# Kernel optimization log

Measured on AMD Instinct MI355X. Metric: run time of the kernel, lower is better.

The kernel has to match this reference:

```python
import jax, jax.numpy as jnp
import numpy as np

N_HEADS = 16
D_QK = 64
D_MODEL = 1024
LN_EPS = 1e-6
B, QL, KVL = 2, 2048, 2048


def rms_norm(x, weight, eps=LN_EPS):
    var = jnp.mean(jnp.square(x.astype(jnp.float32)), axis=-1, keepdims=True)
    return (x * jax.lax.rsqrt(var + eps)).astype(x.dtype) * weight


def setup_inputs() -> dict:
    key = jax.random.key(0)
    ks = jax.random.split(key, 5)
    scale_h = 1.0 / np.sqrt(D_MODEL)
    return {
        "q_hidden_states": jax.random.normal(ks[0], (B, QL, D_MODEL), jnp.float32),
        "q_sequence_mask": jnp.ones((B, QL), dtype=bool),
        "kv_hidden_states": jax.random.normal(ks[1], (B, KVL, D_MODEL), jnp.float32),
        "kv_sequence_mask": jnp.ones((B, KVL), dtype=bool),
        "w_q": jax.random.normal(ks[2], (D_MODEL, N_HEADS * D_QK), jnp.float32) * scale_h,
        "w_kv": jax.random.normal(ks[3], (D_MODEL, 2 * N_HEADS * D_QK), jnp.float32) * scale_h,
        "w_o": jax.random.normal(ks[4], (N_HEADS * D_QK, D_MODEL), jnp.float32) * scale_h,
        "ln_weight": jnp.ones((D_MODEL,), jnp.float32),
    }


def reference(q_hidden_states, q_sequence_mask, kv_hidden_states, kv_sequence_mask,
              w_q, w_kv, w_o, ln_weight):
    b, ql, _ = q_hidden_states.shape
    kvl = kv_hidden_states.shape[1]

    normed = rms_norm(q_hidden_states, ln_weight)

    # q projection: [b, ql, H*D] -> [b, H, ql, D]
    q = (normed @ w_q).reshape(b, ql, N_HEADS, D_QK).transpose(0, 2, 1, 3)
    # kv projection: [b, kvl, 2*H*D] -> k, v each [b, H, kvl, D]
    kv = (kv_hidden_states @ w_kv).reshape(b, kvl, 2, N_HEADS, D_QK)
    k = kv[:, :, 0].transpose(0, 2, 1, 3)
    v = kv[:, :, 1].transpose(0, 2, 1, 3)

    # T5 attention: no 1/sqrt(d) scaling
    scores = jnp.einsum("bhqd,bhkd->bhqk", q, k)  # [b, H, ql, kvl]
    attn_mask = q_sequence_mask[:, None, :, None] & kv_sequence_mask[:, None, None, :]
    scores = jnp.where(attn_mask, scores, jnp.finfo(jnp.float32).min)
    attn = jax.nn.softmax(scores.astype(jnp.float32), axis=-1).astype(q.dtype)

    out = jnp.einsum("bhqk,bhkd->bhqd", attn, v)  # [b, H, ql, D]
    out = out.transpose(0, 2, 1, 3).reshape(b, ql, N_HEADS * D_QK)
    out = out @ w_o
    return q_hidden_states + out
```

## Files before the change

### kernel.cpp

```cpp
#include <hip/hip_runtime.h>
#include <stdint.h>

#define BSZ 2
#define QL 2048
#define KVL 2048
#define NH 16
#define DQK 64
#define DM 1024

typedef __bf16 bf16x8 __attribute__((ext_vector_type(8)));
typedef float f32x4 __attribute__((ext_vector_type(4)));

__device__ __forceinline__ ushort f2bf(float f) {
    union { float f; uint32_t u; } c; c.f = f;
    uint32_t u = c.u;
    return (ushort)((u + 0x7fffu + ((u >> 16) & 1u)) >> 16);
}

__device__ __forceinline__ uint32_t pack2bf(float lo, float hi) {
    union { float f; uint32_t u; } a, b;
    a.f = lo; b.f = hi;
    return __builtin_amdgcn_perm(b.u + 0x8000u, a.u + 0x8000u, 0x07060302u);
}

__device__ __forceinline__ uint32_t pack2bf_t(float lo, float hi) {
    union { float f; uint32_t u; } a, b;
    a.f = lo; b.f = hi;
    return __builtin_amdgcn_perm(b.u, a.u, 0x07060302u);
}

#define GLOAD_LDS16(g, l)                                              \
    __builtin_amdgcn_global_load_lds(                                  \
        (const __attribute__((address_space(1))) uint32_t*)(g),        \
        (__attribute__((address_space(3))) uint32_t*)(l), 16, 0, 0)

__global__ __launch_bounds__(256) void prep_k(const float* __restrict__ qh_in,
                                              const float* __restrict__ lnw,
                                              ushort* __restrict__ normed,
                                              const float* __restrict__ kv_in,
                                              ushort* __restrict__ kvb,
                                              const float* __restrict__ w_q,
                                              const float* __restrict__ w_kv,
                                              const float* __restrict__ w_o,
                                              ushort* __restrict__ wqT,
                                              ushort* __restrict__ wkvT,
                                              ushort* __restrict__ woT) {
    int blk = blockIdx.x;
    int tid = threadIdx.x;
    if (blk < 4096) {
        int row = blk;
        const float4* xr = (const float4*)(qh_in + (size_t)row * DM);
        float4 v = xr[tid];
        float s = v.x * v.x + v.y * v.y + v.z * v.z + v.w * v.w;
#pragma unroll
        for (int off = 32; off > 0; off >>= 1) s += __shfl_down(s, off, 64);
        __shared__ float ws4[4];
        if ((tid & 63) == 0) ws4[tid >> 6] = s;
        __syncthreads();
        float tot = ws4[0] + ws4[1] + ws4[2] + ws4[3];
        float r = rsqrtf(tot * (1.0f / DM) + 1e-6f);
        float4 wv = ((const float4*)lnw)[tid];
        ushort4 o;
        o.x = f2bf(v.x * r * wv.x);
        o.y = f2bf(v.y * r * wv.y);
        o.z = f2bf(v.z * r * wv.z);
        o.w = f2bf(v.w * r * wv.w);
        ((ushort4*)(normed + (size_t)row * DM))[tid] = o;
        return;
    }
    if (blk < 8192) {
        int i = (blk - 4096) * 256 + tid;
        float4 v = ((const float4*)kv_in)[i];
        ushort4 r;
        r.x = f2bf(v.x); r.y = f2bf(v.y); r.z = f2bf(v.z); r.w = f2bf(v.w);
        ((ushort4*)kvb)[i] = r;
        return;
    }
    __shared__ ushort tile[64][65];
    int bi = blk - 8192;
    const float* in; ushort* out; int N, bx, by;
    const int K = 1024;
    if (bi < 256)      { in = w_q;  out = wqT;  N = 1024; bx = bi & 15; by = bi >> 4; }
    else if (bi < 768) { int j = bi - 256; in = w_kv; out = wkvT; N = 2048; bx = j & 31; by = j >> 5; }
    else               { int j = bi - 768; in = w_o;  out = woT;  N = 1024; bx = j & 15; by = j >> 4; }
    int k0 = by * 64, n0 = bx * 64;
    int colBase = tid & 63;
    int rowOff = tid >> 6;
#pragma unroll
    for (int i = 0; i < 16; ++i) {
        int row = i * 4 + rowOff;
        tile[colBase][row] = f2bf(in[(size_t)(k0 + row) * N + n0 + colBase]);
    }
    __syncthreads();
#pragma unroll
    for (int i = 0; i < 16; ++i) {
        int nrow = i * 4 + rowOff;
        out[(size_t)(n0 + nrow) * K + k0 + colBase] = tile[nrow][colBase];
    }
}

__global__ __launch_bounds__(256) void gemm_qkv_k(
    const ushort* __restrict__ normed, const ushort* __restrict__ kvb,
    const ushort* __restrict__ wqT, const ushort* __restrict__ wkvT,
    ushort* __restrict__ q_out, ushort* __restrict__ k_out, ushort* __restrict__ vt_out) {
    __shared__ __align__(16) ushort smem[16896];
    ushort* As = smem;
    ushort* Bs = smem + 4096;
    const int K = DM;
    int tid = threadIdx.x;
    int wave = tid >> 6, lane = tid & 63, quad = lane >> 4, l16 = lane & 15;
    int bx = blockIdx.x;
    int isQ = bx < 8;
    const ushort* A = isQ ? normed : kvb;
    const ushort* Bt = isQ ? wqT : wkvT;
    int n0 = (isQ ? bx : bx - 8) * 128;
    int m0 = blockIdx.y * 128;
    int wm = (wave & 1) * 64, wn = (wave >> 1) * 64;

    int r0 = tid >> 2, c0 = (tid & 3) << 3;
    const ushort* ga0 = &A[(size_t)(m0 + r0) * K + c0];
    const ushort* gb0 = &Bt[(size_t)(n0 + r0) * K + c0];

    f32x4 zero = {0.f, 0.f, 0.f, 0.f};
    f32x4 acc[4][4];
#pragma unroll
    for (int i = 0; i < 4; ++i)
#pragma unroll
        for (int j = 0; j < 4; ++j) acc[i][j] = zero;

    for (int k0 = 0; k0 < K; k0 += 32) {
        GLOAD_LDS16(ga0 + k0, &As[tid * 8]);
        GLOAD_LDS16(ga0 + (size_t)64 * K + k0, &As[(tid + 256) * 8]);
        GLOAD_LDS16(gb0 + k0, &Bs[tid * 8]);
        GLOAD_LDS16(gb0 + (size_t)64 * K + k0, &Bs[(tid + 256) * 8]);
        __syncthreads();
        bf16x8 af[4], bfr[4];
#pragma unroll
        for (int mi = 0; mi < 4; ++mi)
            af[mi] = *(const bf16x8*)(&As[(wm + mi * 16 + l16) * 32 + quad * 8]);
#pragma unroll
        for (int ni = 0; ni < 4; ++ni)
            bfr[ni] = *(const bf16x8*)(&Bs[(wn + ni * 16 + l16) * 32 + quad * 8]);
#pragma unroll
        for (int mi = 0; mi < 4; ++mi)
#pragma unroll
            for (int ni = 0; ni < 4; ++ni)
                acc[mi][ni] = __builtin_amdgcn_mfma_f32_16x16x32_bf16(
                    af[mi], bfr[ni], acc[mi][ni], 0, 0, 0);
        __syncthreads();
    }

    const float L2E = 1.44269504089f;
    int b = m0 >> 11, m0t = m0 & 2047;
    if (bx < 16) {
        float sc = isQ ? L2E : 1.0f;
        ushort* dst0 = isQ ? q_out : k_out;
#pragma unroll
        for (int mi = 0; mi < 4; ++mi) {
            int t_loc = wm + mi * 16 + quad * 4;
#pragma unroll
            for (int ni = 0; ni < 4; ++ni) {
                int n_loc = wn + ni * 16 + l16;
#pragma unroll
                for (int r = 0; r < 4; ++r) {
                    union { float f; uint32_t u; } c;
                    c.f = acc[mi][ni][r] * sc;
                    smem[(t_loc + r) * 132 + n_loc] = (ushort)((c.u + 0x8000u) >> 16);
                }
            }
        }
        __syncthreads();
        int hb = (n0 >> 6) & 15;
#pragma unroll
        for (int it = 0; it < 8; ++it) {
            int idx = it * 256 + tid;
            int t = idx >> 4, ch = (idx & 15) << 3;
            int h = hb + (ch >> 6), d = ch & 63;
            uint4 vv = *(const uint4*)&smem[t * 132 + ch];
            *(uint4*)&dst0[((size_t)((b << 4) | h) * QL + m0t + t) * DQK + d] = vv;
        }
    } else {
        int hbase = (n0 >> 6) & 15;
        int rbase = ((b << 4) | hbase) * 64;
#pragma unroll
        for (int mi = 0; mi < 4; ++mi) {
            int t_loc = wm + mi * 16 + quad * 4;
#pragma unroll
            for (int ni = 0; ni < 4; ++ni) {
                int n_loc = wn + ni * 16 + l16;
                uint2 pk;
                pk.x = pack2bf(acc[mi][ni][0], acc[mi][ni][1]);
                pk.y = pack2bf(acc[mi][ni][2], acc[mi][ni][3]);
                *(uint2*)&smem[n_loc * 132 + t_loc] = pk;
            }
        }
        __syncthreads();
#pragma unroll
        for (int it = 0; it < 8; ++it) {
            int idx = it * 256 + tid;
            int n = idx >> 4, ch = (idx & 15) << 3;
            uint4 vv = *(const uint4*)&smem[n * 132 + ch];
            *(uint4*)&vt_out[((size_t)(rbase + n)) * KVL + m0t + ch] = vv;
        }
    }
}

__global__ __launch_bounds__(256) void gemm_o_k(const ushort* __restrict__ A,
                                                const ushort* __restrict__ Bt,
                                                const float* __restrict__ resid,
                                                float* __restrict__ f_out) {
    __shared__ __align__(16) ushort As[64 * 32];
    __shared__ __align__(16) ushort Bs[128 * 32];
    const int K = DM;
    int tid = threadIdx.x;
    int wave = tid >> 6, lane = tid & 63, quad = lane >> 4, l16 = lane & 15;
    int n0 = blockIdx.x * 128, m0 = blockIdx.y * 64;
    int wm = (wave & 1) * 32, wn = (wave >> 1) * 64;

    int r0 = tid >> 2, c0 = (tid & 3) << 3;
    const ushort* ga0 = &A[(size_t)(m0 + r0) * K + c0];
    const ushort* gb0 = &Bt[(size_t)(n0 + r0) * K + c0];

    f32x4 zero = {0.f, 0.f, 0.f, 0.f};
    f32x4 acc[2][4];
#pragma unroll
    for (int i = 0; i < 2; ++i)
#pragma unroll
        for (int j = 0; j < 4; ++j) acc[i][j] = zero;

    for (int k0 = 0; k0 < K; k0 += 32) {
        GLOAD_LDS16(ga0 + k0, &As[tid * 8]);
        GLOAD_LDS16(gb0 + k0, &Bs[tid * 8]);
        GLOAD_LDS16(gb0 + (size_t)64 * K + k0, &Bs[(tid + 256) * 8]);
        __syncthreads();
        bf16x8 af[2], bfr[4];
#pragma unroll
        for (int mi = 0; mi < 2; ++mi)
            af[mi] = *(const bf16x8*)(&As[(wm + mi * 16 + l16) * 32 + quad * 8]);
#pragma unroll
        for (int ni = 0; ni < 4; ++ni)
            bfr[ni] = *(const bf16x8*)(&Bs[(wn + ni * 16 + l16) * 32 + quad * 8]);
#pragma unroll
        for (int mi = 0; mi < 2; ++mi)
#pragma unroll
            for (int ni = 0; ni < 4; ++ni)
                acc[mi][ni] = __builtin_amdgcn_mfma_f32_16x16x32_bf16(
                    af[mi], bfr[ni], acc[mi][ni], 0, 0, 0);
        __syncthreads();
    }

#pragma unroll
    for (int mi = 0; mi < 2; ++mi) {
#pragma unroll
        for (int ni = 0; ni < 4; ++ni) {
#pragma unroll
            for (int r = 0; r < 4; ++r) {
                int mm = m0 + wm + mi * 16 + quad * 4 + r;
                int nn = n0 + wn + ni * 16 + l16;
                size_t o = (size_t)mm * DM + nn;
                f_out[o] = resid[o] + acc[mi][ni][r];
            }
        }
    }
}

__global__ __launch_bounds__(256) void attn_k(const ushort* __restrict__ qh,
                                              const ushort* __restrict__ kh,
                                              const ushort* __restrict__ vt,
                                              ushort* __restrict__ ao) {
    __shared__ __align__(16) ushort smem[2 * 64 * 72 + 8 * 16 * 72];
    ushort* Ks = smem;
    ushort* Vs = smem + 64 * 72;
    ushort* PsB = smem + 2 * 64 * 72;
    int bh = blockIdx.y, bI = bh >> 4, hI = bh & 15;
    int q0 = blockIdx.x * 128;
    int tid = threadIdx.x, wave = tid >> 6, lane = tid & 63;
    int quad = lane >> 4, l16 = lane & 15;
    const ushort* Qp = qh + (size_t)bh * QL * DQK;
    const ushort* Kp = kh + (size_t)bh * KVL * DQK;
    const ushort* Vp = vt + (size_t)bh * DQK * KVL;

    bf16x8 qf[2][2];
#pragma unroll
    for (int g = 0; g < 2; ++g) {
        const ushort* qrow = Qp + (size_t)(q0 + wave * 32 + g * 16 + l16) * DQK;
        qf[g][0] = *(const bf16x8*)(qrow + quad * 8);
        qf[g][1] = *(const bf16x8*)(qrow + 32 + quad * 8);
    }

    bf16x8 onef;
#pragma unroll
    for (int j = 0; j < 8; ++j) onef[j] = (l16 == 0) ? (__bf16)1.0f : (__bf16)0.0f;

    int srow = tid >> 3;
    int scol = (tid & 7) << 3;

    f32x4 zero = {0.f, 0.f, 0.f, 0.f};
    f32x4 o[2][4];
    f32x4 lacc[2];
#pragma unroll
    for (int g = 0; g < 2; ++g) {
        lacc[g] = zero;
#pragma unroll
        for (int i = 0; i < 4; ++i) o[g][i] = zero;
    }

    uint4 kr0 = *(const uint4*)&Kp[(size_t)srow * DQK + scol];
    uint4 kr1 = *(const uint4*)&Kp[(size_t)(srow + 32) * DQK + scol];
    uint4 vr0 = *(const uint4*)&Vp[(size_t)srow * KVL + scol];
    uint4 vr1 = *(const uint4*)&Vp[(size_t)(srow + 32) * KVL + scol];

    for (int t0 = 0; t0 < KVL; t0 += 64) {
        *(uint4*)&Ks[srow * 72 + scol] = kr0;
        *(uint4*)&Ks[(srow + 32) * 72 + scol] = kr1;
        *(uint4*)&Vs[srow * 72 + scol] = vr0;
        *(uint4*)&Vs[(srow + 32) * 72 + scol] = vr1;
        __syncthreads();
        int tn = t0 + 64;
        if (tn < KVL) {
            kr0 = *(const uint4*)&Kp[(size_t)(tn + srow) * DQK + scol];
            kr1 = *(const uint4*)&Kp[(size_t)(tn + srow + 32) * DQK + scol];
            vr0 = *(const uint4*)&Vp[(size_t)srow * KVL + tn + scol];
            vr1 = *(const uint4*)&Vp[(size_t)(srow + 32) * KVL + tn + scol];
        }

        f32x4 s[2][4];
#pragma unroll
        for (int mi = 0; mi < 4; ++mi) {
            const ushort* kb = &Ks[(mi * 16 + l16) * 72 + quad * 8];
            bf16x8 kf0 = *(const bf16x8*)kb;
            bf16x8 kf1 = *(const bf16x8*)(kb + 32);
#pragma unroll
            for (int g = 0; g < 2; ++g) {
                f32x4 a = zero;
                a = __builtin_amdgcn_mfma_f32_16x16x32_bf16(kf0, qf[g][0], a, 0, 0, 0);
                a = __builtin_amdgcn_mfma_f32_16x16x32_bf16(kf1, qf[g][1], a, 0, 0, 0);
                s[g][mi] = a;
            }
        }

        bf16x8 pf[2][2];
#pragma unroll
        for (int g = 0; g < 2; ++g) {
#pragma unroll
            for (int mi = 0; mi < 4; ++mi)
#pragma unroll
                for (int r = 0; r < 4; ++r)
                    s[g][mi][r] = __builtin_amdgcn_exp2f(s[g][mi][r]);
            ushort* prow = &PsB[((wave * 2 + g) * 16 + l16) * 72];
#pragma unroll
            for (int mi = 0; mi < 4; ++mi) {
                uint2 pk;
                pk.x = pack2bf_t(s[g][mi][0], s[g][mi][1]);
                pk.y = pack2bf_t(s[g][mi][2], s[g][mi][3]);
                *(uint2*)&prow[mi * 16 + quad * 4] = pk;
            }
            pf[g][0] = *(const bf16x8*)&prow[quad * 8];
            pf[g][1] = *(const bf16x8*)&prow[32 + quad * 8];
            lacc[g] = __builtin_amdgcn_mfma_f32_16x16x32_bf16(onef, pf[g][0], lacc[g], 0, 0, 0);
            lacc[g] = __builtin_amdgcn_mfma_f32_16x16x32_bf16(onef, pf[g][1], lacc[g], 0, 0, 0);
        }

#pragma unroll
        for (int mi = 0; mi < 4; ++mi) {
            const ushort* vb = &Vs[(mi * 16 + l16) * 72 + quad * 8];
            bf16x8 vf0 = *(const bf16x8*)vb;
            bf16x8 vf1 = *(const bf16x8*)(vb + 32);
#pragma unroll
            for (int g = 0; g < 2; ++g) {
                o[g][mi] = __builtin_amdgcn_mfma_f32_16x16x32_bf16(vf0, pf[g][0], o[g][mi], 0, 0, 0);
                o[g][mi] = __builtin_amdgcn_mfma_f32_16x16x32_bf16(vf1, pf[g][1], o[g][mi], 0, 0, 0);
            }
        }
        __syncthreads();
    }

#pragma unroll
    for (int g = 0; g < 2; ++g) {
        float lg = lacc[g][0];
        lg += __shfl_xor(lg, 16, 64);
        lg += __shfl_xor(lg, 32, 64);
        float rinv = __builtin_amdgcn_rcpf(lg);
        ushort* orow = &smem[(size_t)(wave * 32 + g * 16 + l16) * 72];
#pragma unroll
        for (int mi = 0; mi < 4; ++mi) {
            uint2 pk;
            pk.x = pack2bf(o[g][mi][0] * rinv, o[g][mi][1] * rinv);
            pk.y = pack2bf(o[g][mi][2] * rinv, o[g][mi][3] * rinv);
            *(uint2*)&orow[mi * 16 + quad * 4] = pk;
        }
    }
    __syncthreads();
#pragma unroll
    for (int it = 0; it < 4; ++it) {
        int idx = tid + it * 256;
        int ql = idx >> 3, c = (idx & 7) << 3;
        uint4 vv = *(const uint4*)&smem[ql * 72 + c];
        *(uint4*)&ao[((size_t)(bI * QL + q0 + ql)) * DM + hI * 64 + c] = vv;
    }
}

extern "C" void kernel_launch(void* const* d_in, const int* in_sizes, int n_in,
                              void* d_out, int out_size, void* d_ws, size_t ws_size,
                              hipStream_t stream) {
    (void)in_sizes; (void)n_in; (void)out_size; (void)ws_size;
    const float* qh_in = (const float*)d_in[0];
    const float* kv_in = (const float*)d_in[2];
    const float* w_q  = (const float*)d_in[4];
    const float* w_kv = (const float*)d_in[5];
    const float* w_o  = (const float*)d_in[6];
    const float* lnw  = (const float*)d_in[7];
    float* out = (float*)d_out;

    char* ws = (char*)d_ws;
    ushort* normed = (ushort*)(ws);
    ushort* kvb    = (ushort*)(ws + ((size_t)8 << 20));
    ushort* wqT    = (ushort*)(ws + ((size_t)16 << 20));
    ushort* wkvT   = (ushort*)(ws + ((size_t)18 << 20));
    ushort* woT    = (ushort*)(ws + ((size_t)22 << 20));
    ushort* qheads = (ushort*)(ws + ((size_t)24 << 20));
    ushort* kheads = (ushort*)(ws + ((size_t)32 << 20));
    ushort* vT     = (ushort*)(ws + ((size_t)40 << 20));
    ushort* attno  = (ushort*)(ws + ((size_t)48 << 20));

    prep_k<<<9216, 256, 0, stream>>>(qh_in, lnw, normed, kv_in, kvb,
                                     w_q, w_kv, w_o, wqT, wkvT, woT);
    gemm_qkv_k<<<dim3(24, 32), 256, 0, stream>>>(normed, kvb, wqT, wkvT,
                                                 qheads, kheads, vT);
    attn_k<<<dim3(QL / 128, BSZ * NH), 256, 0, stream>>>(qheads, kheads, vT, attno);
    gemm_o_k<<<dim3(8, 64), 256, 0, stream>>>(attno, woT, qh_in, out);
}
```

Baseline: 220.7 us.

## Shrink GEMM tiles and keep attention P in registers via 16x16x16 MFMA

Halves the M tile of the QKV projection GEMM and the N tile of the output GEMM, doubling the grid sizes to raise occupancy and wave count. The attention kernel stops staging the softmax P tile through LDS and instead feeds it straight from registers into 16x16x16 bf16 MFMAs, with V fragments preloaded in a layout that matches. This removes the LDS round trip and a barrier-free shuffle. In exchange it issues twice as many smaller MFMAs, and the smaller GEMM tiles reuse less data per block.

Result: slower. 227.1 us (+2.9%).

```diff
diff --git a/kernel.cpp b/kernel.cpp
--- a/kernel.cpp
+++ b/kernel.cpp
@@ -10,6 +10,7 @@
 
 typedef __bf16 bf16x8 __attribute__((ext_vector_type(8)));
 typedef float f32x4 __attribute__((ext_vector_type(4)));
+typedef short short4v __attribute__((ext_vector_type(4)));
 
 __device__ __forceinline__ ushort f2bf(float f) {
     union { float f; uint32_t u; } c; c.f = f;
@@ -27,6 +28,16 @@
     union { float f; uint32_t u; } a, b;
     a.f = lo; b.f = hi;
     return __builtin_amdgcn_perm(b.u, a.u, 0x07060302u);
+}
+
+__device__ __forceinline__ f32x4 mfma16(short4v a, short4v b, f32x4 c) {
+#if __has_builtin(__builtin_amdgcn_mfma_f32_16x16x16bf16_1k)
+    return __builtin_amdgcn_mfma_f32_16x16x16bf16_1k(a, b, c, 0, 0, 0);
+#else
+    asm volatile("v_mfma_f32_16x16x16_bf16 %0, %1, %2, %0"
+                 : "+v"(c) : "v"(a), "v"(b));
+    return c;
+#endif
 }
 
 #define GLOAD_LDS16(g, l)                                              \
@@ -103,9 +114,9 @@
     const ushort* __restrict__ normed, const ushort* __restrict__ kvb,
     const ushort* __restrict__ wqT, const ushort* __restrict__ wkvT,
     ushort* __restrict__ q_out, ushort* __restrict__ k_out, ushort* __restrict__ vt_out) {
-    __shared__ __align__(16) ushort smem[16896];
+    __shared__ __align__(16) ushort smem[9216];
     ushort* As = smem;
-    ushort* Bs = smem + 4096;
+    ushort* Bs = smem + 2048;
     const int K = DM;
     int tid = threadIdx.x;
     int wave = tid >> 6, lane = tid & 63, quad = lane >> 4, l16 = lane & 15;
@@ -114,35 +125,34 @@
     const ushort* A = isQ ? normed : kvb;
     const ushort* Bt = isQ ? wqT : wkvT;
     int n0 = (isQ ? bx : bx - 8) * 128;
-    int m0 = blockIdx.y * 128;
-    int wm = (wave & 1) * 64, wn = (wave >> 1) * 64;
+    int m0 = blockIdx.y * 64;
+    int wm = (wave & 1) * 32, wn = (wave >> 1) * 64;
 
     int r0 = tid >> 2, c0 = (tid & 3) << 3;
     const ushort* ga0 = &A[(size_t)(m0 + r0) * K + c0];
     const ushort* gb0 = &Bt[(size_t)(n0 + r0) * K + c0];
 
     f32x4 zero = {0.f, 0.f, 0.f, 0.f};
-    f32x4 acc[4][4];
-#pragma unroll
-    for (int i = 0; i < 4; ++i)
+    f32x4 acc[2][4];
+#pragma unroll
+    for (int i = 0; i < 2; ++i)
 #pragma unroll
         for (int j = 0; j < 4; ++j) acc[i][j] = zero;
 
     for (int k0 = 0; k0 < K; k0 += 32) {
         GLOAD_LDS16(ga0 + k0, &As[tid * 8]);
-        GLOAD_LDS16(ga0 + (size_t)64 * K + k0, &As[(tid + 256) * 8]);
         GLOAD_LDS16(gb0 + k0, &Bs[tid * 8]);
         GLOAD_LDS16(gb0 + (size_t)64 * K + k0, &Bs[(tid + 256) * 8]);
         __syncthreads();
-        bf16x8 af[4], bfr[4];
-#pragma unroll
-        for (int mi = 0; mi < 4; ++mi)
+        bf16x8 af[2], bfr[4];
+#pragma unroll
+        for (int mi = 0; mi < 2; ++mi)
             af[mi] = *(const bf16x8*)(&As[(wm + mi * 16 + l16) * 32 + quad * 8]);
 #pragma unroll
         for (int ni = 0; ni < 4; ++ni)
             bfr[ni] = *(const bf16x8*)(&Bs[(wn + ni * 16 + l16) * 32 + quad * 8]);
 #pragma unroll
-        for (int mi = 0; mi < 4; ++mi)
+        for (int mi = 0; mi < 2; ++mi)
 #pragma unroll
             for (int ni = 0; ni < 4; ++ni)
                 acc[mi][ni] = __builtin_amdgcn_mfma_f32_16x16x32_bf16(
@@ -156,7 +166,7 @@
         float sc = isQ ? L2E : 1.0f;
         ushort* dst0 = isQ ? q_out : k_out;
 #pragma unroll
-        for (int mi = 0; mi < 4; ++mi) {
+        for (int mi = 0; mi < 2; ++mi) {
             int t_loc = wm + mi * 16 + quad * 4;
 #pragma unroll
             for (int ni = 0; ni < 4; ++ni) {
@@ -165,25 +175,25 @@
                 for (int r = 0; r < 4; ++r) {
                     union { float f; uint32_t u; } c;
                     c.f = acc[mi][ni][r] * sc;
-                    smem[(t_loc + r) * 132 + n_loc] = (ushort)((c.u + 0x8000u) >> 16);
+                    smem[(t_loc + r) * 136 + n_loc] = (ushort)((c.u + 0x8000u) >> 16);
                 }
             }
         }
         __syncthreads();
         int hb = (n0 >> 6) & 15;
 #pragma unroll
-        for (int it = 0; it < 8; ++it) {
+        for (int it = 0; it < 4; ++it) {
             int idx = it * 256 + tid;
             int t = idx >> 4, ch = (idx & 15) << 3;
             int h = hb + (ch >> 6), d = ch & 63;
-            uint4 vv = *(const uint4*)&smem[t * 132 + ch];
+            uint4 vv = *(const uint4*)&smem[t * 136 + ch];
             *(uint4*)&dst0[((size_t)((b << 4) | h) * QL + m0t + t) * DQK + d] = vv;
         }
     } else {
         int hbase = (n0 >> 6) & 15;
         int rbase = ((b << 4) | hbase) * 64;
 #pragma unroll
-        for (int mi = 0; mi < 4; ++mi) {
+        for (int mi = 0; mi < 2; ++mi) {
             int t_loc = wm + mi * 16 + quad * 4;
 #pragma unroll
             for (int ni = 0; ni < 4; ++ni) {
@@ -191,15 +201,15 @@
                 uint2 pk;
                 pk.x = pack2bf(acc[mi][ni][0], acc[mi][ni][1]);
                 pk.y = pack2bf(acc[mi][ni][2], acc[mi][ni][3]);
-                *(uint2*)&smem[n_loc * 132 + t_loc] = pk;
+                *(uint2*)&smem[n_loc * 72 + t_loc] = pk;
             }
         }
         __syncthreads();
 #pragma unroll
-        for (int it = 0; it < 8; ++it) {
+        for (int it = 0; it < 4; ++it) {
             int idx = it * 256 + tid;
-            int n = idx >> 4, ch = (idx & 15) << 3;
-            uint4 vv = *(const uint4*)&smem[n * 132 + ch];
+            int n = idx >> 3, ch = (idx & 7) << 3;
+            uint4 vv = *(const uint4*)&smem[n * 72 + ch];
             *(uint4*)&vt_out[((size_t)(rbase + n)) * KVL + m0t + ch] = vv;
         }
     }
@@ -210,40 +220,39 @@
                                                 const float* __restrict__ resid,
                                                 float* __restrict__ f_out) {
     __shared__ __align__(16) ushort As[64 * 32];
-    __shared__ __align__(16) ushort Bs[128 * 32];
+    __shared__ __align__(16) ushort Bs[64 * 32];
     const int K = DM;
     int tid = threadIdx.x;
     int wave = tid >> 6, lane = tid & 63, quad = lane >> 4, l16 = lane & 15;
-    int n0 = blockIdx.x * 128, m0 = blockIdx.y * 64;
-    int wm = (wave & 1) * 32, wn = (wave >> 1) * 64;
+    int n0 = blockIdx.x * 64, m0 = blockIdx.y * 64;
+    int wm = (wave & 1) * 32, wn = (wave >> 1) * 32;
 
     int r0 = tid >> 2, c0 = (tid & 3) << 3;
     const ushort* ga0 = &A[(size_t)(m0 + r0) * K + c0];
     const ushort* gb0 = &Bt[(size_t)(n0 + r0) * K + c0];
 
     f32x4 zero = {0.f, 0.f, 0.f, 0.f};
-    f32x4 acc[2][4];
+    f32x4 acc[2][2];
 #pragma unroll
     for (int i = 0; i < 2; ++i)
 #pragma unroll
-        for (int j = 0; j < 4; ++j) acc[i][j] = zero;
+        for (int j = 0; j < 2; ++j) acc[i][j] = zero;
 
     for (int k0 = 0; k0 < K; k0 += 32) {
         GLOAD_LDS16(ga0 + k0, &As[tid * 8]);
         GLOAD_LDS16(gb0 + k0, &Bs[tid * 8]);
-        GLOAD_LDS16(gb0 + (size_t)64 * K + k0, &Bs[(tid + 256) * 8]);
-        __syncthreads();
-        bf16x8 af[2], bfr[4];
+        __syncthreads();
+        bf16x8 af[2], bfr[2];
 #pragma unroll
         for (int mi = 0; mi < 2; ++mi)
             af[mi] = *(const bf16x8*)(&As[(wm + mi * 16 + l16) * 32 + quad * 8]);
 #pragma unroll
-        for (int ni = 0; ni < 4; ++ni)
+        for (int ni = 0; ni < 2; ++ni)
             bfr[ni] = *(const bf16x8*)(&Bs[(wn + ni * 16 + l16) * 32 + quad * 8]);
 #pragma unroll
         for (int mi = 0; mi < 2; ++mi)
 #pragma unroll
-            for (int ni = 0; ni < 4; ++ni)
+            for (int ni = 0; ni < 2; ++ni)
                 acc[mi][ni] = __builtin_amdgcn_mfma_f32_16x16x32_bf16(
                     af[mi], bfr[ni], acc[mi][ni], 0, 0, 0);
         __syncthreads();
@@ -252,7 +261,7 @@
 #pragma unroll
     for (int mi = 0; mi < 2; ++mi) {
 #pragma unroll
-        for (int ni = 0; ni < 4; ++ni) {
+        for (int ni = 0; ni < 2; ++ni) {
 #pragma unroll
             for (int r = 0; r < 4; ++r) {
                 int mm = m0 + wm + mi * 16 + quad * 4 + r;
@@ -268,10 +277,9 @@
                                               const ushort* __restrict__ kh,
                                               const ushort* __restrict__ vt,
                                               ushort* __restrict__ ao) {
-    __shared__ __align__(16) ushort smem[2 * 64 * 72 + 8 * 16 * 72];
+    __shared__ __align__(16) ushort smem[9216];
     ushort* Ks = smem;
-    ushort* Vs = smem + 64 * 72;
-    ushort* PsB = smem + 2 * 64 * 72;
+    ushort* Vs = smem + 4608;
     int bh = blockIdx.y, bI = bh >> 4, hI = bh & 15;
     int q0 = blockIdx.x * 128;
     int tid = threadIdx.x, wave = tid >> 6, lane = tid & 63;
@@ -288,9 +296,9 @@
         qf[g][1] = *(const bf16x8*)(qrow + 32 + quad * 8);
     }
 
-    bf16x8 onef;
-#pragma unroll
-    for (int j = 0; j < 8; ++j) onef[j] = (l16 == 0) ? (__bf16)1.0f : (__bf16)0.0f;
+    short4v onef4;
+#pragma unroll
+    for (int j = 0; j < 4; ++j) onef4[j] = (l16 == 0) ? (short)0x3F80 : (short)0;
 
     int srow = tid >> 3;
     int scol = (tid & 7) << 3;
@@ -324,6 +332,13 @@
             vr1 = *(const uint4*)&Vp[(size_t)(srow + 32) * KVL + tn + scol];
         }
 
+        short4v vf[4][4];
+#pragma unroll
+        for (int ni = 0; ni < 4; ++ni)
+#pragma unroll
+            for (int mi = 0; mi < 4; ++mi)
+                vf[ni][mi] = *(const short4v*)&Vs[(ni * 16 + l16) * 72 + mi * 16 + quad * 4];
+
         f32x4 s[2][4];
 #pragma unroll
         for (int mi = 0; mi < 4; ++mi) {
@@ -339,7 +354,6 @@
             }
         }
 
-        bf16x8 pf[2][2];
 #pragma unroll
         for (int g = 0; g < 2; ++g) {
 #pragma unroll
@@ -347,30 +361,22 @@
 #pragma unroll
                 for (int r = 0; r < 4; ++r)
                     s[g][mi][r] = __builtin_amdgcn_exp2f(s[g][mi][r]);
-            ushort* prow = &PsB[((wave * 2 + g) * 16 + l16) * 72];
+            short4v pb[4];
 #pragma unroll
             for (int mi = 0; mi < 4; ++mi) {
-                uint2 pk;
-                pk.x = pack2bf_t(s[g][mi][0], s[g][mi][1]);
-                pk.y = pack2bf_t(s[g][mi][2], s[g][mi][3]);
-                *(uint2*)&prow[mi * 16 + quad * 4] = pk;
+                union { uint2 u; short4v s4; } pk;
+                pk.u.x = pack2bf_t(s[g][mi][0], s[g][mi][1]);
+                pk.u.y = pack2bf_t(s[g][mi][2], s[g][mi][3]);
+                pb[mi] = pk.s4;
             }
-            pf[g][0] = *(const bf16x8*)&prow[quad * 8];
-            pf[g][1] = *(const bf16x8*)&prow[32 + quad * 8];
-            lacc[g] = __builtin_amdgcn_mfma_f32_16x16x32_bf16(onef, pf[g][0], lacc[g], 0, 0, 0);
-            lacc[g] = __builtin_amdgcn_mfma_f32_16x16x32_bf16(onef, pf[g][1], lacc[g], 0, 0, 0);
-        }
-
-#pragma unroll
-        for (int mi = 0; mi < 4; ++mi) {
-            const ushort* vb = &Vs[(mi * 16 + l16) * 72 + quad * 8];
-            bf16x8 vf0 = *(const bf16x8*)vb;
-            bf16x8 vf1 = *(const bf16x8*)(vb + 32);
-#pragma unroll
-            for (int g = 0; g < 2; ++g) {
-                o[g][mi] = __builtin_amdgcn_mfma_f32_16x16x32_bf16(vf0, pf[g][0], o[g][mi], 0, 0, 0);
-                o[g][mi] = __builtin_amdgcn_mfma_f32_16x16x32_bf16(vf1, pf[g][1], o[g][mi], 0, 0, 0);
-            }
+#pragma unroll
+            for (int mi = 0; mi < 4; ++mi)
+                lacc[g] = mfma16(onef4, pb[mi], lacc[g]);
+#pragma unroll
+            for (int ni = 0; ni < 4; ++ni)
+#pragma unroll
+                for (int mi = 0; mi < 4; ++mi)
+                    o[g][ni] = mfma16(vf[ni][mi], pb[mi], o[g][ni]);
         }
         __syncthreads();
     }
@@ -425,8 +431,8 @@
 
     prep_k<<<9216, 256, 0, stream>>>(qh_in, lnw, normed, kv_in, kvb,
                                      w_q, w_kv, w_o, wqT, wkvT, woT);
-    gemm_qkv_k<<<dim3(24, 32), 256, 0, stream>>>(normed, kvb, wqT, wkvT,
+    gemm_qkv_k<<<dim3(24, 64), 256, 0, stream>>>(normed, kvb, wqT, wkvT,
                                                  qheads, kheads, vT);
     attn_k<<<dim3(QL / 128, BSZ * NH), 256, 0, stream>>>(qheads, kheads, vT, attno);
-    gemm_o_k<<<dim3(8, 64), 256, 0, stream>>>(attno, woT, qh_in, out);
-}
+    gemm_o_k<<<dim3(16, 64), 256, 0, stream>>>(attno, woT, qh_in, out);
+}
```
